# Performance work log

Measured on AMD Instinct MI355X. Metric: run time of the kernel, lower is better.

The kernel has to match this reference:

```python
import jax, jax.numpy as jnp
import numpy as np

TEMP = 0.3
LAM = 0.9
NUM_LABELS = 7
B, D = 8192, 768


def setup_inputs() -> dict:
    key = jax.random.key(0)
    k1, k2, k3, k4 = jax.random.split(key, 4)
    cls_emb = jax.random.normal(k1, (B, D), dtype=jnp.float32)
    pooled = jax.random.normal(k2, (B, D), dtype=jnp.float32)
    labels = jax.random.randint(k3, (B,), 0, NUM_LABELS)
    W = jax.random.normal(k4, (NUM_LABELS, D), dtype=jnp.float32) * 0.02
    b = jnp.zeros((NUM_LABELS,), dtype=jnp.float32)
    return {"cls_emb": cls_emb, "pooled": pooled, "labels": labels, "W": W, "b": b}


def reference(cls_emb, pooled, labels, W, b):
    # classifier head (dropout = identity in eval)
    logits = pooled @ W.T + b  # [B, num_labels]

    # cross-entropy (mean reduction, as nn.CrossEntropyLoss default)
    logp = jax.nn.log_softmax(logits, axis=-1)
    ce = -jnp.mean(jnp.take_along_axis(logp, labels[:, None], axis=1)[:, 0])

    # supervised contrastive loss on DETACHED cls embeddings (original uses .detach().numpy())
    e = jax.lax.stop_gradient(cls_emb)
    en = e / jnp.linalg.norm(e, axis=1, keepdims=True)
    S = (en @ en.T) / TEMP  # [B, B] scaled cosine similarity
    n = S.shape[0]
    eye = jnp.eye(n, dtype=bool)
    # row_sum excludes the diagonal -> stable off-diagonal logsumexp
    lse = jax.nn.logsumexp(jnp.where(eye, -jnp.inf, S), axis=1)  # [B]
    pos = (labels[:, None] == labels[None, :]) & ~eye  # [B, B]
    n_i = jnp.sum(pos, axis=1).astype(S.dtype)  # positives per anchor
    inner = jnp.sum(jnp.where(pos, S - lse[:, None], 0.0), axis=1)  # sum log(exp(s)/row_sum)
    per_anchor = jnp.where(n_i > 0, -inner / jnp.maximum(n_i, 1.0), 0.0)
    contrastive = jnp.sum(per_anchor)  # summed over anchors, as in original

    loss = LAM * contrastive + (1.0 - LAM) * ce
    return loss, logits
```

## Files before the change

kernel.cpp:

```cpp
#include <hip/hip_runtime.h>
#include <hip/hip_bf16.h>


#define B_N 8192
#define D_K 768
#define NLAB 7
#define MBOUND 3.3333333333333335f
#define RTINV 1.8257418583505538f

typedef float f32x4 __attribute__((ext_vector_type(4)));
typedef int i32x8 __attribute__((ext_vector_type(8)));

__device__ __forceinline__ void gl2lds16(const void* g, void* l) {
  __builtin_amdgcn_global_load_lds(
      (const __attribute__((address_space(1))) void*)g,
      (__attribute__((address_space(3))) void*)l, 16, 0, 0);
}

__device__ __forceinline__ float bf16u_to_f(unsigned short u) {
  return __uint_as_float(((unsigned int)u) << 16);
}

__device__ __forceinline__ float dec8(unsigned int b) {
  unsigned int s = (b >> 7) & 1u, e = (b >> 3) & 15u, m = b & 7u;
  float fn = __uint_as_float((s << 31) | ((e + 120u) << 23) | (m << 20));
  float fs = (s ? -1.f : 1.f) * (float)m * 0.001953125f;
  return e ? fn : fs;
}

template <int WBF>
__global__ __launch_bounds__(256) void k_prep(
    const float* __restrict__ cls, const float* __restrict__ pooled,
    const int* __restrict__ labels, const float* __restrict__ W,
    const float* __restrict__ bias, unsigned char* __restrict__ e8,
    unsigned short* __restrict__ en, float* __restrict__ logits_out,
    float* __restrict__ celoss, int* __restrict__ zr) {
  if (blockIdx.x == 0)
    for (int t = threadIdx.x; t < 9280; t += 256) zr[t] = 0;

  int wv = threadIdx.x >> 6, lane = threadIdx.x & 63;
  int row = blockIdx.x * 4 + wv;

  const float4* src = (const float4*)(cls + (size_t)row * D_K);
  float4 x[3];
  float ss = 0.f;
#pragma unroll
  for (int j = 0; j < 3; ++j) {
    x[j] = src[j * 64 + lane];
    ss += x[j].x * x[j].x + x[j].y * x[j].y + x[j].z * x[j].z + x[j].w * x[j].w;
  }
#pragma unroll
  for (int m = 1; m < 64; m <<= 1) ss += __shfl_xor(ss, m);
  float sc = rsqrtf(ss) * RTINV;
  int* d8 = (int*)(e8 + (size_t)row * D_K);
  ushort4* db = (ushort4*)(en + (size_t)row * D_K);
#pragma unroll
  for (int j = 0; j < 3; ++j) {
    int w32 = __builtin_amdgcn_cvt_pk_fp8_f32(x[j].x * sc, x[j].y * sc, 0, false);
    w32 = __builtin_amdgcn_cvt_pk_fp8_f32(x[j].z * sc, x[j].w * sc, w32, true);
    d8[j * 64 + lane] = w32;
    if (WBF) {
      const float* xv = reinterpret_cast<const float*>(&x[j]);
      ushort4 o;
      unsigned short* ov = reinterpret_cast<unsigned short*>(&o);
#pragma unroll
      for (int k = 0; k < 4; ++k) {
        __hip_bfloat16 h = __float2bfloat16(xv[k] * sc);
        ov[k] = *reinterpret_cast<unsigned short*>(&h);
      }
      db[j * 64 + lane] = o;
    }
  }

  const float4* p4 = (const float4*)(pooled + (size_t)row * D_K);
  float acc[NLAB];
#pragma unroll
  for (int c = 0; c < NLAB; ++c) acc[c] = 0.f;
#pragma unroll
  for (int j = 0; j < 3; ++j) {
    float4 xx = p4[j * 64 + lane];
#pragma unroll
    for (int c = 0; c < NLAB; ++c) {
      float4 w = ((const float4*)(W + c * D_K))[j * 64 + lane];
      acc[c] += xx.x * w.x + xx.y * w.y + xx.z * w.z + xx.w * w.w;
    }
  }
#pragma unroll
  for (int c = 0; c < NLAB; ++c)
#pragma unroll
    for (int m = 1; m < 64; m <<= 1) acc[c] += __shfl_xor(acc[c], m);
  if (lane == 0) {
    float l[NLAB], mx = -1e30f;
#pragma unroll
    for (int c = 0; c < NLAB; ++c) { l[c] = acc[c] + bias[c]; mx = fmaxf(mx, l[c]); }
    float se = 0.f;
#pragma unroll
    for (int c = 0; c < NLAB; ++c) se += __expf(l[c] - mx);
    float lse = mx + __logf(se);
    celoss[row] = lse - l[labels[row]];
    float* o = logits_out + (size_t)row * NLAB;
#pragma unroll
    for (int c = 0; c < NLAB; ++c) o[c] = l[c];
  }
}

template <int M>
__global__ __launch_bounds__(256) void k_classumA(
    const unsigned short* __restrict__ en, const unsigned char* __restrict__ e8,
    const int* __restrict__ labels, float* __restrict__ partial,
    int* __restrict__ hist) {
  int g = blockIdx.x, t = threadIdx.x;
  int r0 = g * 128;
  if (t < 192) {
    float acc[NLAB][4];
#pragma unroll
    for (int c = 0; c < NLAB; ++c)
#pragma unroll
      for (int k = 0; k < 4; ++k) acc[c][k] = 0.f;
    for (int r = 0; r < 128; r += 4) {
      int lab[4];
      float xv[4][4];
#pragma unroll
      for (int q = 0; q < 4; ++q) {
        int row = r0 + r + q;
        lab[q] = labels[row];
        if (M == 0) {
          ushort4 u = *(const ushort4*)(en + (size_t)row * D_K + t * 4);
          xv[q][0] = bf16u_to_f(u.x); xv[q][1] = bf16u_to_f(u.y);
          xv[q][2] = bf16u_to_f(u.z); xv[q][3] = bf16u_to_f(u.w);
        } else {
          uchar4 u = *(const uchar4*)(e8 + (size_t)row * D_K + t * 4);
          xv[q][0] = dec8(u.x); xv[q][1] = dec8(u.y);
          xv[q][2] = dec8(u.z); xv[q][3] = dec8(u.w);
        }
      }
#pragma unroll
      for (int q = 0; q < 4; ++q)
#pragma unroll
        for (int c = 0; c < NLAB; ++c) {
          bool m = (lab[q] == c);
          acc[c][0] += m ? xv[q][0] : 0.f;
          acc[c][1] += m ? xv[q][1] : 0.f;
          acc[c][2] += m ? xv[q][2] : 0.f;
          acc[c][3] += m ? xv[q][3] : 0.f;
        }
    }
    float* dst = partial + (size_t)g * (NLAB * D_K);
#pragma unroll
    for (int c = 0; c < NLAB; ++c) {
      float4 v = {acc[c][0], acc[c][1], acc[c][2], acc[c][3]};
      *(float4*)(dst + c * D_K + t * 4) = v;
    }
  } else {
    int lane = t - 192;
    int cnt[NLAB];
#pragma unroll
    for (int c = 0; c < NLAB; ++c) cnt[c] = 0;
#pragma unroll
    for (int q = 0; q < 2; ++q) {
      int lab = labels[r0 + q * 64 + lane];
#pragma unroll
      for (int c = 0; c < NLAB; ++c) cnt[c] += (lab == c);
    }
#pragma unroll
    for (int c = 0; c < NLAB; ++c)
#pragma unroll
      for (int m = 1; m < 64; m <<= 1) cnt[c] += __shfl_xor(cnt[c], m);
    if (lane == 0)
#pragma unroll
      for (int c = 0; c < NLAB; ++c) atomicAdd(&hist[c], cnt[c]);
  }
}

__global__ __launch_bounds__(256) void k_scl(const unsigned char* __restrict__ e8,
                                             float* __restrict__ rse,
                                             const float* __restrict__ partial,
                                             float* __restrict__ T) {
  if (blockIdx.x >= 2080) {
    int idx = (int)(blockIdx.x - 2080) * 256 + threadIdx.x;
    float v = 0.f;
    for (int g = 0; g < 64; ++g) v += partial[(size_t)g * (NLAB * D_K) + idx];
    T[idx] = v;
    return;
  }
  __shared__ __align__(16) unsigned char As[128 * 128];
  __shared__ __align__(16) unsigned char Bs[128 * 128];

  int rem = blockIdx.x;
  int BI = 0, BJ = 0;
  for (;;) {
    int sz = (BI == BJ) ? 36 : 64;
    if (rem < sz) break;
    rem -= sz;
    if (++BJ == 8) { ++BI; BJ = BI; }
  }
  int bi, bj;
  if (BI == BJ) {
    int r = 0, w = 8;
    while (rem >= w) { rem -= w; ++r; --w; }
    bi = BI * 8 + r;
    bj = BJ * 8 + r + rem;
  } else {
    bi = BI * 8 + (rem >> 3);
    bj = BJ * 8 + (rem & 7);
  }

  const int i0 = bi * 128, j0 = bj * 128;
  const int tid = threadIdx.x, wv = tid >> 6, lane = tid & 63;
  const int quad = lane >> 4, cix = lane & 15;
  const int rowTile = 64 * (wv >> 1), colTile = 64 * (wv & 1);

  f32x4 acc[4][4] = {};

  for (int kc = 0; kc < 6; ++kc) {
    __syncthreads();
#pragma unroll
    for (int it = 0; it < 4; ++it) {
      int s = it * 256 + tid;
      int r = s >> 3;
      int p = ((s & 7) - r) & 7;
      int lbase = (it * 256 + wv * 64) * 16;
      gl2lds16(e8 + (size_t)(i0 + r) * D_K + kc * 128 + p * 16, (char*)As + lbase);
      gl2lds16(e8 + (size_t)(j0 + r) * D_K + kc * 128 + p * 16, (char*)Bs + lbase);
    }
    __syncthreads();
    i32x8 aF[4];
#pragma unroll
    for (int mt = 0; mt < 4; ++mt) {
      int r = rowTile + 16 * mt + cix;
      const char* base = (const char*)As + r * 128;
      int4 lo = *(const int4*)(base + (((quad * 2 + 0) + r) & 7) * 16);
      int4 hi = *(const int4*)(base + (((quad * 2 + 1) + r) & 7) * 16);
      aF[mt][0] = lo.x; aF[mt][1] = lo.y; aF[mt][2] = lo.z; aF[mt][3] = lo.w;
      aF[mt][4] = hi.x; aF[mt][5] = hi.y; aF[mt][6] = hi.z; aF[mt][7] = hi.w;
    }
#pragma unroll
    for (int nt = 0; nt < 4; ++nt) {
      int r = colTile + 16 * nt + cix;
      const char* base = (const char*)Bs + r * 128;
      int4 lo = *(const int4*)(base + (((quad * 2 + 0) + r) & 7) * 16);
      int4 hi = *(const int4*)(base + (((quad * 2 + 1) + r) & 7) * 16);
      i32x8 bF;
      bF[0] = lo.x; bF[1] = lo.y; bF[2] = lo.z; bF[3] = lo.w;
      bF[4] = hi.x; bF[5] = hi.y; bF[6] = hi.z; bF[7] = hi.w;
#pragma unroll
      for (int mt = 0; mt < 4; ++mt)
        acc[mt][nt] = __builtin_amdgcn_mfma_scale_f32_16x16x128_f8f6f4(
            aF[mt], bF, acc[mt][nt], 0, 0, 0, 127, 0, 127);
    }
  }

  if (bi != bj) {
    float ce_col[4] = {0.f, 0.f, 0.f, 0.f};
#pragma unroll
    for (int mt = 0; mt < 4; ++mt) {
      int rowbase = i0 + rowTile + 16 * mt + quad * 4;
      float rs_e[4] = {0.f, 0.f, 0.f, 0.f};
#pragma unroll
      for (int nt = 0; nt < 4; ++nt) {
#pragma unroll
        for (int rg = 0; rg < 4; ++rg) {
          float e = __expf(acc[mt][nt][rg] - MBOUND);
          rs_e[rg] += e;
          ce_col[nt] += e;
        }
      }
#pragma unroll
      for (int rg = 0; rg < 4; ++rg)
#pragma unroll
        for (int m = 1; m <= 8; m <<= 1) rs_e[rg] += __shfl_xor(rs_e[rg], m);
      if (cix == 0)
#pragma unroll
        for (int rg = 0; rg < 4; ++rg) atomicAdd(&rse[rowbase + rg], rs_e[rg]);
    }
#pragma unroll
    for (int nt = 0; nt < 4; ++nt) {
      ce_col[nt] += __shfl_xor(ce_col[nt], 16);
      ce_col[nt] += __shfl_xor(ce_col[nt], 32);
    }
    if (quad == 0)
#pragma unroll
      for (int nt = 0; nt < 4; ++nt)
        atomicAdd(&rse[j0 + colTile + 16 * nt + cix], ce_col[nt]);
  } else {
#pragma unroll
    for (int mt = 0; mt < 4; ++mt) {
      int rowbase = i0 + rowTile + 16 * mt + quad * 4;
      float rs_e[4] = {0.f, 0.f, 0.f, 0.f};
#pragma unroll
      for (int nt = 0; nt < 4; ++nt) {
        int gcol = j0 + colTile + 16 * nt + cix;
#pragma unroll
        for (int rg = 0; rg < 4; ++rg) {
          bool dg = (rowbase + rg) == gcol;
          rs_e[rg] += dg ? 0.f : __expf(acc[mt][nt][rg] - MBOUND);
        }
      }
#pragma unroll
      for (int rg = 0; rg < 4; ++rg)
#pragma unroll
        for (int m = 1; m <= 8; m <<= 1) rs_e[rg] += __shfl_xor(rs_e[rg], m);
      if (cix == 0)
#pragma unroll
        for (int rg = 0; rg < 4; ++rg) atomicAdd(&rse[rowbase + rg], rs_e[rg]);
    }
  }
}

template <int M>
__global__ __launch_bounds__(256) void k_rowfinal(
    const float* __restrict__ rse, const unsigned short* __restrict__ en,
    const unsigned char* __restrict__ e8, const float* __restrict__ T,
    const int* __restrict__ labels, const int* __restrict__ hist,
    const float* __restrict__ celoss, float* __restrict__ contrP,
    int* __restrict__ done_count, float* __restrict__ out) {
  __shared__ float part[4];
  int wv = threadIdx.x >> 6, lane = threadIdx.x & 63;
  int row = blockIdx.x * 4 + wv;
  int l = labels[row];
  const float4* t4 = (const float4*)(T + (size_t)l * D_K);
  float pd = 0.f, sd = 0.f;
#pragma unroll
  for (int j = 0; j < 3; ++j) {
    float a0, a1, a2, a3;
    if (M == 0) {
      ushort4 u = ((const ushort4*)(en + (size_t)row * D_K))[j * 64 + lane];
      a0 = bf16u_to_f(u.x); a1 = bf16u_to_f(u.y);
      a2 = bf16u_to_f(u.z); a3 = bf16u_to_f(u.w);
    } else {
      uint u = ((const uint*)(e8 + (size_t)row * D_K))[j * 64 + lane];
      a0 = dec8(u & 0xff); a1 = dec8((u >> 8) & 0xff);
      a2 = dec8((u >> 16) & 0xff); a3 = dec8(u >> 24);
    }
    float4 t = t4[j * 64 + lane];
    pd += a0 * t.x + a1 * t.y + a2 * t.z + a3 * t.w;
    sd += a0 * a0 + a1 * a1 + a2 * a2 + a3 * a3;
  }
#pragma unroll
  for (int m = 1; m < 64; m <<= 1) {
    pd += __shfl_xor(pd, m);
    sd += __shfl_xor(sd, m);
  }
  if (lane == 0) {
    int ni = hist[l] - 1;
    float per = 0.f;
    if (ni > 0) per = MBOUND + __logf(rse[row]) - (pd - sd) / (float)ni;
    part[wv] = 0.9f * per + (0.1f / (float)B_N) * celoss[row];
  }
  __syncthreads();
  if (threadIdx.x == 0) {
    float v = part[0] + part[1] + part[2] + part[3];
    atomicAdd(&contrP[(blockIdx.x & 63) * 16], v);
    __threadfence();
    int n = atomicAdd(done_count, 1);
    if (n == (int)gridDim.x - 1) {
      float s = 0.f;
      for (int i = 0; i < 64; ++i)
        s += __hip_atomic_load(&contrP[i * 16], __ATOMIC_RELAXED,
                               __HIP_MEMORY_SCOPE_AGENT);
      out[0] = s;
    }
  }
}

extern "C" void kernel_launch(void* const* d_in, const int* in_sizes, int n_in,
                              void* d_out, int out_size, void* d_ws, size_t ws_size,
                              hipStream_t stream) {
  const float* cls    = (const float*)d_in[0];
  const float* pooled = (const float*)d_in[1];
  const int*   labels = (const int*)d_in[2];
  const float* W      = (const float*)d_in[3];
  const float* bias   = (const float*)d_in[4];
  float* out = (float*)d_out;

  char* ws = (char*)d_ws;
  unsigned char* e8 = (unsigned char*)ws;
  const size_t EN_B = (size_t)B_N * D_K * 2;
  const size_t E8_B = (size_t)B_N * D_K;
  size_t need_big = E8_B + EN_B + 98304 + 64 * (size_t)(NLAB * D_K) * 4;
  bool big = ws_size >= need_big;
  unsigned short* en = (unsigned short*)(ws + E8_B);
  size_t off = big ? (E8_B + EN_B) : E8_B;
  float* rse     = (float*)(ws + off);
  int*   hist    = (int*)(ws + off + 32768);
  int*   done    = (int*)(ws + off + 32896);
  float* contrP  = (float*)(ws + off + 33024);
  float* T       = (float*)(ws + off + 37120);
  float* celoss  = (float*)(ws + off + 58624);
  float* partial = (float*)(ws + off + 98304);
  int*   zr      = (int*)(ws + off);

  if (big)
    k_prep<1><<<B_N / 4, 256, 0, stream>>>(cls, pooled, labels, W, bias, e8, en,
                                           out + 1, celoss, zr);
  else
    k_prep<0><<<B_N / 4, 256, 0, stream>>>(cls, pooled, labels, W, bias, e8, en,
                                           out + 1, celoss, zr);
  if (big)
    k_classumA<0><<<64, 256, 0, stream>>>(en, e8, labels, partial, hist);
  else
    k_classumA<1><<<64, 256, 0, stream>>>(en, e8, labels, partial, hist);
  k_scl<<<2101, 256, 0, stream>>>(e8, rse, partial, T);
  if (big)
    k_rowfinal<0><<<B_N / 4, 256, 0, stream>>>(rse, en, e8, T, labels, hist,
                                               celoss, contrP, done, out);
  else
    k_rowfinal<1><<<B_N / 4, 256, 0, stream>>>(rse, en, e8, T, labels, hist,
                                               celoss, contrP, done, out);
}
```

Before: 224.9 us.

## Double-buffer LDS tiles in SCL GEMM and split class-sum over feature halves

The similarity GEMM kernel now uses two LDS buffers per operand. The next K-chunk is prefetched with global_load_lds while MFMAs run on the current chunk, and a single barrier per iteration replaces the previous pair. Global offsets are precomputed once. The class-sum kernel now launches twice as many blocks, each covering half the feature dimension with 96 active threads, to spread the work across more CUs. LDS use per block doubles, which may reduce occupancy.

```diff
diff --git a/kernel.cpp b/kernel.cpp
--- a/kernel.cpp
+++ b/kernel.cpp
@@ -110,8 +110,10 @@
     const int* __restrict__ labels, float* __restrict__ partial,
     int* __restrict__ hist) {
   int g = blockIdx.x, t = threadIdx.x;
-  int r0 = g * 128;
-  if (t < 192) {
+  int slab = g >> 1, half = g & 1;
+  int r0 = slab * 128;
+  int dbase = half * 384;
+  if (t < 96) {
     float acc[NLAB][4];
 #pragma unroll
     for (int c = 0; c < NLAB; ++c)
@@ -125,11 +127,11 @@
         int row = r0 + r + q;
         lab[q] = labels[row];
         if (M == 0) {
-          ushort4 u = *(const ushort4*)(en + (size_t)row * D_K + t * 4);
+          ushort4 u = *(const ushort4*)(en + (size_t)row * D_K + dbase + t * 4);
           xv[q][0] = bf16u_to_f(u.x); xv[q][1] = bf16u_to_f(u.y);
           xv[q][2] = bf16u_to_f(u.z); xv[q][3] = bf16u_to_f(u.w);
         } else {
-          uchar4 u = *(const uchar4*)(e8 + (size_t)row * D_K + t * 4);
+          uchar4 u = *(const uchar4*)(e8 + (size_t)row * D_K + dbase + t * 4);
           xv[q][0] = dec8(u.x); xv[q][1] = dec8(u.y);
           xv[q][2] = dec8(u.z); xv[q][3] = dec8(u.w);
         }
@@ -145,13 +147,13 @@
           acc[c][3] += m ? xv[q][3] : 0.f;
         }
     }
-    float* dst = partial + (size_t)g * (NLAB * D_K);
+    float* dst = partial + (size_t)slab * (NLAB * D_K) + dbase;
 #pragma unroll
     for (int c = 0; c < NLAB; ++c) {
       float4 v = {acc[c][0], acc[c][1], acc[c][2], acc[c][3]};
       *(float4*)(dst + c * D_K + t * 4) = v;
     }
-  } else {
+  } else if (t >= 192 && half == 0) {
     int lane = t - 192;
     int cnt[NLAB];
 #pragma unroll
@@ -183,8 +185,8 @@
     T[idx] = v;
     return;
   }
-  __shared__ __align__(16) unsigned char As[128 * 128];
-  __shared__ __align__(16) unsigned char Bs[128 * 128];
+  __shared__ __align__(16) unsigned char As[2][128 * 128];
+  __shared__ __align__(16) unsigned char Bs[2][128 * 128];
 
   int rem = blockIdx.x;
   int BI = 0, BJ = 0;
@@ -210,25 +212,45 @@
   const int quad = lane >> 4, cix = lane & 15;
   const int rowTile = 64 * (wv >> 1), colTile = 64 * (wv & 1);
 
+  int aoff[4], boff[4], lbase[4];
+#pragma unroll
+  for (int it = 0; it < 4; ++it) {
+    int s = it * 256 + tid;
+    int r = s >> 3;
+    int p = ((s & 7) - r) & 7;
+    aoff[it] = (i0 + r) * D_K + p * 16;
+    boff[it] = (j0 + r) * D_K + p * 16;
+    lbase[it] = (it * 256 + wv * 64) * 16;
+  }
+
   f32x4 acc[4][4] = {};
 
+#pragma unroll
+  for (int it = 0; it < 4; ++it) {
+    gl2lds16(e8 + (size_t)aoff[it], (char*)As[0] + lbase[it]);
+    gl2lds16(e8 + (size_t)boff[it], (char*)Bs[0] + lbase[it]);
+  }
+
+#pragma unroll
   for (int kc = 0; kc < 6; ++kc) {
-    __syncthreads();
-#pragma unroll
-    for (int it = 0; it < 4; ++it) {
-      int s = it * 256 + tid;
-      int r = s >> 3;
-      int p = ((s & 7) - r) & 7;
-      int lbase = (it * 256 + wv * 64) * 16;
-      gl2lds16(e8 + (size_t)(i0 + r) * D_K + kc * 128 + p * 16, (char*)As + lbase);
-      gl2lds16(e8 + (size_t)(j0 + r) * D_K + kc * 128 + p * 16, (char*)Bs + lbase);
-    }
-    __syncthreads();
+    const int cb = kc & 1;
+    __builtin_amdgcn_sched_barrier(0);
+    asm volatile("s_waitcnt vmcnt(0)" ::: "memory");
+    __builtin_amdgcn_s_barrier();
+    asm volatile("" ::: "memory");
+    if (kc < 5) {
+#pragma unroll
+      for (int it = 0; it < 4; ++it) {
+        gl2lds16(e8 + (size_t)(aoff[it] + (kc + 1) * 128), (char*)As[cb ^ 1] + lbase[it]);
+        gl2lds16(e8 + (size_t)(boff[it] + (kc + 1) * 128), (char*)Bs[cb ^ 1] + lbase[it]);
+      }
+    }
+    asm volatile("" ::: "memory");
     i32x8 aF[4];
 #pragma unroll
     for (int mt = 0; mt < 4; ++mt) {
       int r = rowTile + 16 * mt + cix;
-      const char* base = (const char*)As + r * 128;
+      const char* base = (const char*)As[cb] + r * 128;
       int4 lo = *(const int4*)(base + (((quad * 2 + 0) + r) & 7) * 16);
       int4 hi = *(const int4*)(base + (((quad * 2 + 1) + r) & 7) * 16);
       aF[mt][0] = lo.x; aF[mt][1] = lo.y; aF[mt][2] = lo.z; aF[mt][3] = lo.w;
@@ -237,7 +259,7 @@
 #pragma unroll
     for (int nt = 0; nt < 4; ++nt) {
       int r = colTile + 16 * nt + cix;
-      const char* base = (const char*)Bs + r * 128;
+      const char* base = (const char*)Bs[cb] + r * 128;
       int4 lo = *(const int4*)(base + (((quad * 2 + 0) + r) & 7) * 16);
       int4 hi = *(const int4*)(base + (((quad * 2 + 1) + r) & 7) * 16);
       i32x8 bF;
@@ -397,9 +419,9 @@
     k_prep<0><<<B_N / 4, 256, 0, stream>>>(cls, pooled, labels, W, bias, e8, en,
                                            out + 1, celoss, zr);
   if (big)
-    k_classumA<0><<<64, 256, 0, stream>>>(en, e8, labels, partial, hist);
+    k_classumA<0><<<128, 256, 0, stream>>>(en, e8, labels, partial, hist);
   else
-    k_classumA<1><<<64, 256, 0, stream>>>(en, e8, labels, partial, hist);
+    k_classumA<1><<<128, 256, 0, stream>>>(en, e8, labels, partial, hist);
   k_scl<<<2101, 256, 0, stream>>>(e8, rse, partial, T);
   if (big)
     k_rowfinal<0><<<B_N / 4, 256, 0, stream>>>(rse, en, e8, T, labels, hist,
```

Result: no change. 225.3 us (+0.2%).
